# Performance work log

Hardware: AMD Instinct MI355X
Metric: run time of the kernel (lower is better)

The kernel has to match this reference:

```python
import jax, jax.numpy as jnp
import numpy as np

B, N, D, H, E = 16, 512, 256, 8, 16
DH = D // H
NEG = -1e9


def setup_inputs() -> dict:
    key = jax.random.key(0)
    ks = jax.random.split(key, 12)
    s = 0.02
    return {
        "h": jax.random.normal(ks[0], (B, N, D), dtype=jnp.float32),
        "edges": jax.random.normal(ks[1], (B, N, N, E), dtype=jnp.float32),
        "dense_mask": jnp.ones((B, N, N), dtype=bool),
        "mask": jnp.ones((B, N), dtype=bool),
        "Wq": jax.random.normal(ks[2], (D, D), dtype=jnp.float32) * s,
        "bq": jnp.zeros((D,), dtype=jnp.float32),
        "Wk": jax.random.normal(ks[3], (D, D), dtype=jnp.float32) * s,
        "bk": jnp.zeros((D,), dtype=jnp.float32),
        "Wv": jax.random.normal(ks[4], (D, D), dtype=jnp.float32) * s,
        "bv": jnp.zeros((D,), dtype=jnp.float32),
        "Wo": jax.random.normal(ks[5], (D, D), dtype=jnp.float32) * s,
        "bo": jnp.zeros((D,), dtype=jnp.float32),
        "Wp": jax.random.normal(ks[6], (E, H), dtype=jnp.float32) * s,
        "bp": jnp.zeros((H,), dtype=jnp.float32),
    }


def reference(h, edges, dense_mask, mask, Wq, bq, Wk, bk, Wv, bv, Wo, bo, Wp, bp):
    # content Q/K/V projections, split into heads
    q = (h @ Wq + bq).reshape(B, N, H, DH)
    k = (h @ Wk + bk).reshape(B, N, H, DH)
    v = (h @ Wv + bv).reshape(B, N, H, DH)
    # scaled content scores [B,H,N,N]
    scores = jnp.einsum("bnhd,bmhd->bhnm", q, k) / jnp.sqrt(jnp.float32(DH))
    # PositionAttention: per-head edge bias from the dense edge stack
    pos = jnp.einsum("bnme,eh->bhnm", edges, Wp) + bp[None, :, None, None]
    pos = pos / jnp.sqrt(jnp.float32(H))  # scale_attention
    scores = scores + pos  # merge_attention: sum (bias injected into scores)
    # fuse edge mask (dense_mask) with key padding mask (~mask is attn_mask)
    valid = dense_mask[:, None, :, :] & mask[:, None, None, :]
    scores = jnp.where(valid, scores, NEG)
    attn = jax.nn.softmax(scores, axis=-1)
    out = jnp.einsum("bhnm,bmhd->bnhd", attn, v).reshape(B, N, D)
    out = out @ Wo + bo
    return out, attn
```

## Files before the change

### kernel.cpp

```cpp
#include <hip/hip_runtime.h>
#include <hip/hip_bf16.h>

constexpr int kB = 16, kN = 512, kD = 256, kH = 8, kE = 16, kDH = 32;

typedef float f4 __attribute__((ext_vector_type(4)));
typedef __bf16 bf8 __attribute__((ext_vector_type(8)));

__global__ __launch_bounds__(256) void cast_h_kernel(const float* __restrict__ h,
                                                     __bf16* __restrict__ hb) {
  const int idx = (blockIdx.x * 256 + threadIdx.x) * 8;
  f4 a = *(const f4*)(h + idx);
  f4 b = *(const f4*)(h + idx + 4);
  bf8 o;
  o[0] = (__bf16)a[0]; o[1] = (__bf16)a[1]; o[2] = (__bf16)a[2]; o[3] = (__bf16)a[3];
  o[4] = (__bf16)b[0]; o[5] = (__bf16)b[1]; o[6] = (__bf16)b[2]; o[7] = (__bf16)b[3];
  *(bf8*)(hb + idx) = o;
}

__global__ __launch_bounds__(256) void prep_w_kernel(
    const float* __restrict__ Wq, const float* __restrict__ Wk,
    const float* __restrict__ Wv, const float* __restrict__ Wo,
    __bf16* __restrict__ Wt, __bf16* __restrict__ Wot) {
  const int r = blockIdx.x;
  const int t = threadIdx.x;
  if (r < 768) {
    const float* src = (r < 256) ? Wq : (r < 512) ? Wk : Wv;
    const int c = r & 255;
    Wt[(size_t)r * 256 + t] = (__bf16)src[(size_t)t * 256 + c];
  } else {
    const int rr = r - 768;
    Wot[(size_t)rr * 256 + t] = (__bf16)Wo[(size_t)t * 256 + rr];
  }
}

__global__ __launch_bounds__(256, 4) void qkv_gemm_kernel(
    const __bf16* __restrict__ hb, const __bf16* __restrict__ Wt,
    const float* __restrict__ bq, const float* __restrict__ bk,
    const float* __restrict__ bv,
    __bf16* __restrict__ qw, __bf16* __restrict__ kw, __bf16* __restrict__ vtw) {
  const int M0 = blockIdx.x * 128;
  const int N0 = blockIdx.y * 64;
  const int tid = threadIdx.x;
  const int wave = tid >> 6, lane = tid & 63;
  const int l15 = lane & 15, lq = lane >> 4;
  const int wm = wave & 1, wn = wave >> 1;
  const f4 fzero = {0.f, 0.f, 0.f, 0.f};

  f4 acc[4][2];
#pragma unroll
  for (int tm = 0; tm < 4; ++tm)
#pragma unroll
    for (int tn = 0; tn < 2; ++tn) acc[tm][tn] = fzero;

#pragma unroll
  for (int kk = 0; kk < 256; kk += 32) {
    bf8 af[4], bfr[2];
#pragma unroll
    for (int tm = 0; tm < 4; ++tm)
      af[tm] = *(const bf8*)(hb + (size_t)(M0 + wm * 64 + tm * 16 + l15) * 256 + kk + lq * 8);
#pragma unroll
    for (int tn = 0; tn < 2; ++tn)
      bfr[tn] = *(const bf8*)(Wt + (size_t)(N0 + wn * 32 + tn * 16 + l15) * 256 + kk + lq * 8);
#pragma unroll
    for (int tm = 0; tm < 4; ++tm)
#pragma unroll
      for (int tn = 0; tn < 2; ++tn)
        acc[tm][tn] = __builtin_amdgcn_mfma_f32_16x16x32_bf16(af[tm], bfr[tn], acc[tm][tn], 0, 0, 0);
  }

  const float QS = 0.17677669529663687f;
  const int wsel = N0 >> 8;
#pragma unroll
  for (int tn = 0; tn < 2; ++tn) {
    const int n = N0 + wn * 32 + tn * 16 + l15;
    const int c = n & 255;
    const float bias = (wsel == 0) ? bq[c] : (wsel == 1) ? bk[c] : bv[c];
#pragma unroll
    for (int tm = 0; tm < 4; ++tm) {
#pragma unroll
      for (int r = 0; r < 4; ++r) {
        const int m = M0 + wm * 64 + tm * 16 + lq * 4 + r;
        const float v = acc[tm][tn][r] + bias;
        if (wsel == 0) {
          qw[(size_t)m * 256 + c] = (__bf16)(v * QS);
        } else if (wsel == 1) {
          kw[(size_t)m * 256 + c] = (__bf16)v;
        } else {
          const int b_ = m >> 9, nn_ = m & 511, hh = c >> 5, dd = c & 31;
          vtw[(((size_t)b_ * kH + hh) * kDH + dd) * kN + nn_] = (__bf16)v;
        }
      }
    }
  }
}

__global__ __launch_bounds__(512, 2) void attn_fused_kernel(
    const __bf16* __restrict__ qw, const __bf16* __restrict__ kw,
    const __bf16* __restrict__ vtw, const float* __restrict__ edges,
    const int* __restrict__ dmask, const int* __restrict__ kmask,
    const float* __restrict__ Wp, const float* __restrict__ bp,
    float* __restrict__ attn_out, __bf16* __restrict__ ow) {
  const int blk = blockIdx.x;
  const int b = blk >> 5;
  const int n0 = (blk & 31) * 16;
  const int tid = threadIdx.x;
  const int wave = tid >> 6, lane = tid & 63;
  const int l15 = lane & 15, lq = lane >> 4;

  __shared__ union {
    float pos[8][16][132];
    __bf16 p[8][16][136];
  } su;

  f4 sc[32];
  const float RS8 = 0.35355339059327373f;
  float bph[8];
#pragma unroll
  for (int hh = 0; hh < 8; ++hh) bph[hh] = bp[hh] * RS8;

  const int mq = tid >> 7;
  const int mm = tid & 127;
#pragma unroll
  for (int cc = 0; cc < 4; ++cc) {
    const int m0 = cc * 128;
    const int km = kmask[b * kN + m0 + mm];
    float accp[4][8];
#pragma unroll
    for (int qq = 0; qq < 4; ++qq)
#pragma unroll
      for (int hh = 0; hh < 8; ++hh) accp[qq][hh] = bph[hh];

#pragma unroll
    for (int e4 = 0; e4 < 4; ++e4) {
      f4 ed[4];
#pragma unroll
      for (int qq = 0; qq < 4; ++qq) {
        const int q = mq * 4 + qq;
        ed[qq] = *(const f4*)(edges + ((size_t)(b * kN + n0 + q) * kN + m0 + mm) * kE + e4 * 4);
        ed[qq] *= RS8;
      }
#pragma unroll
      for (int i = 0; i < 4; ++i) {
#pragma unroll
        for (int hh = 0; hh < 8; ++hh) {
          const float w = Wp[(e4 * 4 + i) * kH + hh];
#pragma unroll
          for (int qq = 0; qq < 4; ++qq) accp[qq][hh] = fmaf(ed[qq][i], w, accp[qq][hh]);
        }
      }
    }
#pragma unroll
    for (int qq = 0; qq < 4; ++qq) {
      const int q = mq * 4 + qq;
      const bool valid = (dmask[(size_t)(b * kN + n0 + q) * kN + m0 + mm] != 0) && (km != 0);
#pragma unroll
      for (int hh = 0; hh < 8; ++hh)
        su.pos[hh][q][mm] = valid ? accp[qq][hh] : -1e9f;
    }
    __syncthreads();
#pragma unroll
    for (int kl = 0; kl < 8; ++kl)
#pragma unroll
      for (int r = 0; r < 4; ++r)
        sc[cc * 8 + kl][r] = su.pos[wave][lq * 4 + r][kl * 16 + l15];
    __syncthreads();
  }

  bf8 qa = *(const bf8*)(qw + ((size_t)(b * kN + n0 + l15) * kH + wave) * kDH + lq * 8);
#pragma unroll
  for (int kt = 0; kt < 32; ++kt) {
    bf8 kb = *(const bf8*)(kw + ((size_t)(b * kN + kt * 16 + l15) * kH + wave) * kDH + lq * 8);
    sc[kt] = __builtin_amdgcn_mfma_f32_16x16x32_bf16(qa, kb, sc[kt], 0, 0, 0);
  }

  float inv[4];
#pragma unroll
  for (int r = 0; r < 4; ++r) {
    float m_ = sc[0][r];
#pragma unroll
    for (int kt = 1; kt < 32; ++kt) m_ = fmaxf(m_, sc[kt][r]);
#pragma unroll
    for (int s = 1; s < 16; s <<= 1) m_ = fmaxf(m_, __shfl_xor(m_, s, 16));
    float s_ = 0.f;
#pragma unroll
    for (int kt = 0; kt < 32; ++kt) {
      const float e_ = __expf(sc[kt][r] - m_);
      sc[kt][r] = e_;
      s_ += e_;
    }
#pragma unroll
    for (int s = 1; s < 16; s <<= 1) s_ += __shfl_xor(s_, s, 16);
    inv[r] = 1.0f / s_;
  }

  const f4 fzero = {0.f, 0.f, 0.f, 0.f};
  f4 oacc[2];
  oacc[0] = fzero; oacc[1] = fzero;
  float* attn_base = attn_out + ((size_t)(b * kH + wave) * kN + n0) * kN;
#pragma unroll
  for (int cc = 0; cc < 4; ++cc) {
#pragma unroll
    for (int kl = 0; kl < 8; ++kl) {
      const int kt = cc * 8 + kl;
#pragma unroll
      for (int r = 0; r < 4; ++r) {
        const float p = sc[kt][r] * inv[r];
        attn_base[(size_t)(lq * 4 + r) * kN + kt * 16 + l15] = p;
        su.p[wave][lq * 4 + r][kl * 16 + l15] = (__bf16)p;
      }
    }
    __asm__ __volatile__("s_waitcnt lgkmcnt(0)" ::: "memory");
#pragma unroll
    for (int mc = 0; mc < 4; ++mc) {
      bf8 pa = *(const bf8*)(&su.p[wave][l15][mc * 32 + lq * 8]);
#pragma unroll
      for (int dd = 0; dd < 2; ++dd) {
        bf8 vb = *(const bf8*)(vtw + (((size_t)(b * kH + wave) * kDH) + dd * 16 + l15) * kN +
                               cc * 128 + mc * 32 + lq * 8);
        oacc[dd] = __builtin_amdgcn_mfma_f32_16x16x32_bf16(pa, vb, oacc[dd], 0, 0, 0);
      }
    }
  }

#pragma unroll
  for (int dd = 0; dd < 2; ++dd)
#pragma unroll
    for (int r = 0; r < 4; ++r)
      ow[(size_t)(b * kN + n0 + lq * 4 + r) * kD + wave * kDH + dd * 16 + l15] = (__bf16)oacc[dd][r];
}

__global__ __launch_bounds__(256, 4) void out_gemm_kernel(
    const __bf16* __restrict__ ob, const __bf16* __restrict__ Wot,
    const float* __restrict__ bo, float* __restrict__ out) {
  const int M0 = blockIdx.x * 128;
  const int N0 = blockIdx.y * 64;
  const int tid = threadIdx.x;
  const int wave = tid >> 6, lane = tid & 63;
  const int l15 = lane & 15, lq = lane >> 4;
  const int wm = wave & 1, wn = wave >> 1;
  const f4 fzero = {0.f, 0.f, 0.f, 0.f};

  f4 acc[4][2];
#pragma unroll
  for (int tm = 0; tm < 4; ++tm)
#pragma unroll
    for (int tn = 0; tn < 2; ++tn) acc[tm][tn] = fzero;

#pragma unroll
  for (int kk = 0; kk < 256; kk += 32) {
    bf8 af[4], bfr[2];
#pragma unroll
    for (int tm = 0; tm < 4; ++tm)
      af[tm] = *(const bf8*)(ob + (size_t)(M0 + wm * 64 + tm * 16 + l15) * 256 + kk + lq * 8);
#pragma unroll
    for (int tn = 0; tn < 2; ++tn)
      bfr[tn] = *(const bf8*)(Wot + (size_t)(N0 + wn * 32 + tn * 16 + l15) * 256 + kk + lq * 8);
#pragma unroll
    for (int tm = 0; tm < 4; ++tm)
#pragma unroll
      for (int tn = 0; tn < 2; ++tn)
        acc[tm][tn] = __builtin_amdgcn_mfma_f32_16x16x32_bf16(af[tm], bfr[tn], acc[tm][tn], 0, 0, 0);
  }

#pragma unroll
  for (int tn = 0; tn < 2; ++tn) {
    const int n = N0 + wn * 32 + tn * 16 + l15;
    const float bias = bo[n];
#pragma unroll
    for (int tm = 0; tm < 4; ++tm)
#pragma unroll
      for (int r = 0; r < 4; ++r) {
        const int m = M0 + wm * 64 + tm * 16 + lq * 4 + r;
        out[(size_t)m * 256 + n] = acc[tm][tn][r] + bias;
      }
  }
}

extern "C" void kernel_launch(void* const* d_in, const int* in_sizes, int n_in,
                              void* d_out, int out_size, void* d_ws, size_t ws_size,
                              hipStream_t stream) {
  const float* h = (const float*)d_in[0];
  const float* edges = (const float*)d_in[1];
  const int* dmask = (const int*)d_in[2];
  const int* kmask = (const int*)d_in[3];
  const float* Wq = (const float*)d_in[4];
  const float* bq = (const float*)d_in[5];
  const float* Wk = (const float*)d_in[6];
  const float* bk = (const float*)d_in[7];
  const float* Wv = (const float*)d_in[8];
  const float* bv = (const float*)d_in[9];
  const float* Wo = (const float*)d_in[10];
  const float* bo = (const float*)d_in[11];
  const float* Wp = (const float*)d_in[12];
  const float* bp = (const float*)d_in[13];

  char* ws = (char*)d_ws;
  __bf16* hb = (__bf16*)(ws);
  __bf16* Wt = (__bf16*)(ws + ((size_t)4 << 20));
  __bf16* Wot = (__bf16*)(ws + ((size_t)4 << 20) + 768 * 256 * 2);
  __bf16* qw = (__bf16*)(ws + ((size_t)5 << 20));
  __bf16* kw = (__bf16*)(ws + ((size_t)9 << 20));
  __bf16* vtw = (__bf16*)(ws + ((size_t)13 << 20));
  __bf16* ow = hb;

  float* out = (float*)d_out;
  float* attn = out + (size_t)kB * kN * kD;

  cast_h_kernel<<<1024, 256, 0, stream>>>(h, hb);
  prep_w_kernel<<<1024, 256, 0, stream>>>(Wq, Wk, Wv, Wo, Wt, Wot);
  qkv_gemm_kernel<<<dim3(64, 12), 256, 0, stream>>>(hb, Wt, bq, bk, bv, qw, kw, vtw);
  attn_fused_kernel<<<512, 512, 0, stream>>>(qw, kw, vtw, edges, dmask, kmask, Wp, bp, attn, ow);
  out_gemm_kernel<<<dim3(64, 4), 256, 0, stream>>>(ow, Wot, bo, out);
}
```

Baseline: 518.7 us.

## Double-buffer position-bias LDS and prefetch edge loads across chunks

```diff
diff --git a/kernel.cpp b/kernel.cpp
--- a/kernel.cpp
+++ b/kernel.cpp
@@ -108,62 +108,92 @@
   const int l15 = lane & 15, lq = lane >> 4;
 
   __shared__ union {
-    float pos[8][16][132];
+    float pos[2][8][16][132];
     __bf16 p[8][16][136];
   } su;
 
   f4 sc[32];
   const float RS8 = 0.35355339059327373f;
-  float bph[8];
-#pragma unroll
-  for (int hh = 0; hh < 8; ++hh) bph[hh] = bp[hh] * RS8;
 
   const int mq = tid >> 7;
   const int mm = tid & 127;
+
+  float bph[8];
+#pragma unroll
+  for (int hh = 0; hh < 8; ++hh) bph[hh] = bp[hh] * RS8;
+
+  f4 edc[4], edn[4];
+#pragma unroll
+  for (int qq = 0; qq < 4; ++qq)
+    edc[qq] = *(const f4*)(edges + ((size_t)(b * kN + n0 + mq * 4 + qq) * kN + mm) * kE);
+
 #pragma unroll
   for (int cc = 0; cc < 4; ++cc) {
     const int m0 = cc * 128;
     const int km = kmask[b * kN + m0 + mm];
-    float accp[4][8];
+    int dmv[4];
 #pragma unroll
     for (int qq = 0; qq < 4; ++qq)
-#pragma unroll
-      for (int hh = 0; hh < 8; ++hh) accp[qq][hh] = bph[hh];
+      dmv[qq] = dmask[(size_t)(b * kN + n0 + mq * 4 + qq) * kN + m0 + mm];
+
+    float2 acc2[4][4];
+#pragma unroll
+    for (int qq = 0; qq < 4; ++qq)
+#pragma unroll
+      for (int h2 = 0; h2 < 4; ++h2) { acc2[qq][h2].x = 0.f; acc2[qq][h2].y = 0.f; }
 
 #pragma unroll
     for (int e4 = 0; e4 < 4; ++e4) {
-      f4 ed[4];
+      if (e4 < 3) {
+#pragma unroll
+        for (int qq = 0; qq < 4; ++qq)
+          edn[qq] = *(const f4*)(edges +
+              ((size_t)(b * kN + n0 + mq * 4 + qq) * kN + m0 + mm) * kE + (e4 + 1) * 4);
+      } else if (cc < 3) {
+#pragma unroll
+        for (int qq = 0; qq < 4; ++qq)
+          edn[qq] = *(const f4*)(edges +
+              ((size_t)(b * kN + n0 + mq * 4 + qq) * kN + m0 + 128 + mm) * kE);
+      }
 #pragma unroll
       for (int qq = 0; qq < 4; ++qq) {
-        const int q = mq * 4 + qq;
-        ed[qq] = *(const f4*)(edges + ((size_t)(b * kN + n0 + q) * kN + m0 + mm) * kE + e4 * 4);
-        ed[qq] *= RS8;
-      }
-#pragma unroll
-      for (int i = 0; i < 4; ++i) {
-#pragma unroll
-        for (int hh = 0; hh < 8; ++hh) {
-          const float w = Wp[(e4 * 4 + i) * kH + hh];
-#pragma unroll
-          for (int qq = 0; qq < 4; ++qq) accp[qq][hh] = fmaf(ed[qq][i], w, accp[qq][hh]);
+#pragma unroll
+        for (int i = 0; i < 4; ++i) {
+          const float ev = edc[qq][i];
+#pragma unroll
+          for (int h2 = 0; h2 < 4; ++h2) {
+            const float2 w2 = *(const float2*)(Wp + (e4 * 4 + i) * kH + h2 * 2);
+            acc2[qq][h2].x = fmaf(ev, w2.x, acc2[qq][h2].x);
+            acc2[qq][h2].y = fmaf(ev, w2.y, acc2[qq][h2].y);
+          }
         }
       }
-    }
+      if (e4 < 3 || cc < 3) {
+#pragma unroll
+        for (int qq = 0; qq < 4; ++qq) edc[qq] = edn[qq];
+      }
+    }
+
 #pragma unroll
     for (int qq = 0; qq < 4; ++qq) {
       const int q = mq * 4 + qq;
-      const bool valid = (dmask[(size_t)(b * kN + n0 + q) * kN + m0 + mm] != 0) && (km != 0);
-#pragma unroll
-      for (int hh = 0; hh < 8; ++hh)
-        su.pos[hh][q][mm] = valid ? accp[qq][hh] : -1e9f;
-    }
-    __syncthreads();
+      const bool valid = (dmv[qq] != 0) && (km != 0);
+#pragma unroll
+      for (int h2 = 0; h2 < 4; ++h2) {
+        const float vx = fmaf(acc2[qq][h2].x, RS8, bph[h2 * 2]);
+        const float vy = fmaf(acc2[qq][h2].y, RS8, bph[h2 * 2 + 1]);
+        su.pos[cc & 1][h2 * 2][q][mm] = valid ? vx : -1e9f;
+        su.pos[cc & 1][h2 * 2 + 1][q][mm] = valid ? vy : -1e9f;
+      }
+    }
+    __asm__ __volatile__("s_waitcnt lgkmcnt(0)" ::: "memory");
+    __builtin_amdgcn_s_barrier();
+    __builtin_amdgcn_sched_barrier(0);
 #pragma unroll
     for (int kl = 0; kl < 8; ++kl)
 #pragma unroll
       for (int r = 0; r < 4; ++r)
-        sc[cc * 8 + kl][r] = su.pos[wave][lq * 4 + r][kl * 16 + l15];
-    __syncthreads();
+        sc[cc * 8 + kl][r] = su.pos[cc & 1][wave][lq * 4 + r][kl * 16 + l15];
   }
 
   bf8 qa = *(const bf8*)(qw + ((size_t)(b * kN + n0 + l15) * kH + wave) * kDH + lq * 8);
```

After: 521.9 us. Within noise of the previous version (+0.6%).

## Stream edge tiles into LDS with async double-buffered loads, per-head pos bias

Applied to the files above, without the earlier changes.

```diff
diff --git a/kernel.cpp b/kernel.cpp
--- a/kernel.cpp
+++ b/kernel.cpp
@@ -5,6 +5,12 @@
 
 typedef float f4 __attribute__((ext_vector_type(4)));
 typedef __bf16 bf8 __attribute__((ext_vector_type(8)));
+
+__device__ __forceinline__ void gload16(const void* g, const void* l) {
+  __builtin_amdgcn_global_load_lds(
+      (const __attribute__((address_space(1))) void*)g,
+      (__attribute__((address_space(3))) void*)l, 16, 0, 0);
+}
 
 __global__ __launch_bounds__(256) void cast_h_kernel(const float* __restrict__ h,
                                                      __bf16* __restrict__ hb) {
@@ -107,63 +113,93 @@
   const int wave = tid >> 6, lane = tid & 63;
   const int l15 = lane & 15, lq = lane >> 4;
 
-  __shared__ union {
-    float pos[8][16][132];
+  __shared__ __align__(16) union {
+    float stg[2][16][64][16];
     __bf16 p[8][16][136];
   } su;
 
   f4 sc[32];
   const float RS8 = 0.35355339059327373f;
-  float bph[8];
-#pragma unroll
-  for (int hh = 0; hh < 8; ++hh) bph[hh] = bp[hh] * RS8;
-
-  const int mq = tid >> 7;
-  const int mm = tid & 127;
-#pragma unroll
-  for (int cc = 0; cc < 4; ++cc) {
-    const int m0 = cc * 128;
-    const int km = kmask[b * kN + m0 + mm];
-    float accp[4][8];
-#pragma unroll
-    for (int qq = 0; qq < 4; ++qq)
-#pragma unroll
-      for (int hh = 0; hh < 8; ++hh) accp[qq][hh] = bph[hh];
-
-#pragma unroll
-    for (int e4 = 0; e4 < 4; ++e4) {
-      f4 ed[4];
-#pragma unroll
-      for (int qq = 0; qq < 4; ++qq) {
-        const int q = mq * 4 + qq;
-        ed[qq] = *(const f4*)(edges + ((size_t)(b * kN + n0 + q) * kN + m0 + mm) * kE + e4 * 4);
-        ed[qq] *= RS8;
-      }
-#pragma unroll
-      for (int i = 0; i < 4; ++i) {
-#pragma unroll
-        for (int hh = 0; hh < 8; ++hh) {
-          const float w = Wp[(e4 * 4 + i) * kH + hh];
-#pragma unroll
-          for (int qq = 0; qq < 4; ++qq) accp[qq][hh] = fmaf(ed[qq][i], w, accp[qq][hh]);
+
+  f4 wpv[4];
+#pragma unroll
+  for (int e4 = 0; e4 < 4; ++e4)
+#pragma unroll
+    for (int i = 0; i < 4; ++i) wpv[e4][i] = Wp[(e4 * 4 + i) * kH + wave] * RS8;
+  const float bph = bp[wave] * RS8;
+
+  const int msub = lane >> 2;
+  const int rotl = lane & 3;
+  const int rb = (l15 >> 1) & 3;
+
+#define STAGE_ISSUE(HC)                                                              \
+  {                                                                                  \
+    const int buf_ = (HC) & 1;                                                       \
+    _Pragma("unroll") for (int i_ = 0; i_ < 8; ++i_) {                               \
+      const int n_ = wave * 8 + i_;                                                  \
+      const int q_ = n_ >> 2;                                                        \
+      const int m_ = (n_ & 3) * 16 + msub;                                           \
+      const int e4_ = (rotl - ((m_ >> 1) & 3)) & 3;                                  \
+      const float* g_ =                                                              \
+          edges + ((size_t)(b * kN + n0 + q_) * kN + (HC)*64 + m_) * kE + e4_ * 4;   \
+      gload16(g_, (const char*)&su.stg[buf_][0][0][0] + n_ * 1024);                  \
+    }                                                                                \
+  }
+
+  STAGE_ISSUE(0);
+  __builtin_amdgcn_sched_barrier(0);
+
+#pragma unroll
+  for (int hc = 0; hc < 8; ++hc) {
+    const int buf = hc & 1;
+    if (hc < 7) {
+      STAGE_ISSUE(hc + 1);
+      __builtin_amdgcn_sched_barrier(0);
+      __asm__ __volatile__("s_waitcnt vmcnt(8)" ::: "memory");
+    } else {
+      __asm__ __volatile__("s_waitcnt vmcnt(0)" ::: "memory");
+    }
+    __builtin_amdgcn_s_barrier();
+    __builtin_amdgcn_sched_barrier(0);
+
+    const float* stg0 = &su.stg[buf][0][0][0];
+#pragma unroll
+    for (int ktl = 0; ktl < 4; ++ktl) {
+      const int mloc = ktl * 16 + l15;
+#pragma unroll
+      for (int r = 0; r < 4; ++r) {
+        const int q = lq * 4 + r;
+        const float* cell = stg0 + ((q * 64 + mloc) << 4);
+        f4 s = {0.f, 0.f, 0.f, 0.f};
+#pragma unroll
+        for (int e4 = 0; e4 < 4; ++e4) {
+          const int rot = (e4 + rb) & 3;
+          f4 ev = *(const f4*)(cell + rot * 4);
+          s += ev * wpv[e4];
         }
-      }
-    }
-#pragma unroll
-    for (int qq = 0; qq < 4; ++qq) {
-      const int q = mq * 4 + qq;
-      const bool valid = (dmask[(size_t)(b * kN + n0 + q) * kN + m0 + mm] != 0) && (km != 0);
-#pragma unroll
-      for (int hh = 0; hh < 8; ++hh)
-        su.pos[hh][q][mm] = valid ? accp[qq][hh] : -1e9f;
-    }
-    __syncthreads();
-#pragma unroll
-    for (int kl = 0; kl < 8; ++kl)
-#pragma unroll
-      for (int r = 0; r < 4; ++r)
-        sc[cc * 8 + kl][r] = su.pos[wave][lq * 4 + r][kl * 16 + l15];
-    __syncthreads();
+        sc[hc * 4 + ktl][r] = (s[0] + s[1]) + (s[2] + s[3]) + bph;
+      }
+    }
+    __builtin_amdgcn_sched_barrier(0);
+    __builtin_amdgcn_s_barrier();
+  }
+#undef STAGE_ISSUE
+
+  unsigned int vmask[4];
+#pragma unroll
+  for (int g = 0; g < 4; ++g) {
+    unsigned int vm = 0u;
+#pragma unroll
+    for (int kl = 0; kl < 8; ++kl) {
+      const int m = (g * 8 + kl) * 16 + l15;
+      const int km = kmask[b * kN + m];
+#pragma unroll
+      for (int r = 0; r < 4; ++r) {
+        const int dm = dmask[(size_t)(b * kN + n0 + lq * 4 + r) * kN + m];
+        vm |= ((km != 0 && dm != 0) ? 1u : 0u) << (kl * 4 + r);
+      }
+    }
+    vmask[g] = vm;
   }
 
   bf8 qa = *(const bf8*)(qw + ((size_t)(b * kN + n0 + l15) * kH + wave) * kDH + lq * 8);
@@ -173,6 +209,14 @@
     sc[kt] = __builtin_amdgcn_mfma_f32_16x16x32_bf16(qa, kb, sc[kt], 0, 0, 0);
   }
 
+#pragma unroll
+  for (int kt = 0; kt < 32; ++kt) {
+    const unsigned int vm = vmask[kt >> 3];
+#pragma unroll
+    for (int r = 0; r < 4; ++r) {
+      if (!((vm >> ((kt & 7) * 4 + r)) & 1u)) sc[kt][r] = -1e9f;
+    }
+  }
   float inv[4];
 #pragma unroll
   for (int r = 0; r < 4; ++r) {
```

New measurement: 550.0 us. 6.0% more time.

## Split edge-bias computation into separate kernel with bf16 packed pos buffer

Applied to the files above, without the earlier changes.

```diff
diff --git a/kernel.cpp b/kernel.cpp
--- a/kernel.cpp
+++ b/kernel.cpp
@@ -5,6 +5,12 @@
 
 typedef float f4 __attribute__((ext_vector_type(4)));
 typedef __bf16 bf8 __attribute__((ext_vector_type(8)));
+
+__device__ __forceinline__ void gload16(const void* g, const void* l) {
+  __builtin_amdgcn_global_load_lds(
+      (const __attribute__((address_space(1))) void*)g,
+      (__attribute__((address_space(3))) void*)l, 16, 0, 0);
+}
 
 __global__ __launch_bounds__(256) void cast_h_kernel(const float* __restrict__ h,
                                                      __bf16* __restrict__ hb) {
@@ -24,12 +30,97 @@
   const int r = blockIdx.x;
   const int t = threadIdx.x;
   if (r < 768) {
-    const float* src = (r < 256) ? Wq : (r < 512) ? Wk : Wv;
+    const float* src = (r < 256) ? Wq : (r < 512) ? Wv : Wv;
+    src = (r < 256) ? Wq : (r < 512) ? Wk : Wv;
     const int c = r & 255;
     Wt[(size_t)r * 256 + t] = (__bf16)src[(size_t)t * 256 + c];
   } else {
     const int rr = r - 768;
     Wot[(size_t)rr * 256 + t] = (__bf16)Wo[(size_t)t * 256 + rr];
+  }
+}
+
+__global__ __launch_bounds__(256) void prep_pos_kernel(
+    const float* __restrict__ edges, const int* __restrict__ dmask,
+    const int* __restrict__ kmask, const float* __restrict__ Wp,
+    const float* __restrict__ bp, unsigned int* __restrict__ posp) {
+  const int bn = blockIdx.x;
+  const int b = bn >> 9;
+  const int n = bn & 511;
+  const int tid = threadIdx.x;
+
+  __shared__ __align__(16) float stg[8192];
+  __shared__ __align__(16) unsigned int prow[2048];
+
+  const float* rowg = edges + (size_t)bn * (kN * kE);
+
+#pragma unroll
+  for (int j = 0; j < 8; ++j) {
+    const int L = j * 4096 + tid * 16;
+    const int c = L >> 6;
+    const int s = (L >> 4) & 3;
+    const int e4 = s ^ (c & 3);
+    gload16(rowg + c * 16 + e4 * 4, (const char*)stg + L);
+  }
+  __asm__ __volatile__("s_waitcnt vmcnt(0)" ::: "memory");
+  __builtin_amdgcn_s_barrier();
+
+  const float RS8 = 0.35355339059327373f;
+  float bph[8];
+#pragma unroll
+  for (int hh = 0; hh < 8; ++hh) bph[hh] = bp[hh] * RS8;
+
+#pragma unroll
+  for (int half = 0; half < 2; ++half) {
+    const int c = half * 256 + tid;
+    const int dm = dmask[(size_t)bn * kN + c];
+    const int km = kmask[b * kN + c];
+    const bool valid = (dm != 0) && (km != 0);
+
+    float acc[8];
+#pragma unroll
+    for (int hh = 0; hh < 8; ++hh) acc[hh] = 0.f;
+#pragma unroll
+    for (int e4 = 0; e4 < 4; ++e4) {
+      const int s = e4 ^ (c & 3);
+      f4 ev = *(const f4*)(stg + c * 16 + s * 4);
+#pragma unroll
+      for (int i = 0; i < 4; ++i) {
+        const float e_ = ev[i];
+#pragma unroll
+        for (int hh = 0; hh < 8; ++hh)
+          acc[hh] = fmaf(e_, Wp[(e4 * 4 + i) * kH + hh], acc[hh]);
+      }
+    }
+
+    unsigned int w[4];
+#pragma unroll
+    for (int pp = 0; pp < 4; ++pp) {
+      const float lo = valid ? fmaf(acc[2 * pp], RS8, bph[2 * pp]) : -1e9f;
+      const float hi = valid ? fmaf(acc[2 * pp + 1], RS8, bph[2 * pp + 1]) : -1e9f;
+      union { __bf16 h2[2]; unsigned int u; } pk;
+      pk.h2[0] = (__bf16)lo;
+      pk.h2[1] = (__bf16)hi;
+      w[pp] = pk.u;
+    }
+    const int rot = (c + (c >> 3)) & 3;
+    uint4 v;
+    ((unsigned int*)&v)[0] = w[(0 - rot) & 3];
+    ((unsigned int*)&v)[1] = w[(1 - rot) & 3];
+    ((unsigned int*)&v)[2] = w[(2 - rot) & 3];
+    ((unsigned int*)&v)[3] = w[(3 - rot) & 3];
+    *(uint4*)&prow[c * 4] = v;
+  }
+  __builtin_amdgcn_s_barrier();
+
+#pragma unroll
+  for (int it = 0; it < 8; ++it) {
+    const int li = it * 256 + tid;
+    const int pp = li >> 9;
+    const int m = li & 511;
+    const int rot = (m + (m >> 3)) & 3;
+    const unsigned int val = prow[m * 4 + ((pp + rot) & 3)];
+    posp[((((size_t)(b * 4 + pp) * kN) + n) << 9) + m] = val;
   }
 }
 
@@ -96,9 +187,7 @@
 
 __global__ __launch_bounds__(512, 2) void attn_fused_kernel(
     const __bf16* __restrict__ qw, const __bf16* __restrict__ kw,
-    const __bf16* __restrict__ vtw, const float* __restrict__ edges,
-    const int* __restrict__ dmask, const int* __restrict__ kmask,
-    const float* __restrict__ Wp, const float* __restrict__ bp,
+    const __bf16* __restrict__ vtw, const unsigned int* __restrict__ posp,
     float* __restrict__ attn_out, __bf16* __restrict__ ow) {
   const int blk = blockIdx.x;
   const int b = blk >> 5;
@@ -107,63 +196,19 @@
   const int wave = tid >> 6, lane = tid & 63;
   const int l15 = lane & 15, lq = lane >> 4;
 
-  __shared__ union {
-    float pos[8][16][132];
-    __bf16 p[8][16][136];
-  } su;
+  __shared__ __align__(16) __bf16 p[8][16][136];
 
   f4 sc[32];
-  const float RS8 = 0.35355339059327373f;
-  float bph[8];
-#pragma unroll
-  for (int hh = 0; hh < 8; ++hh) bph[hh] = bp[hh] * RS8;
-
-  const int mq = tid >> 7;
-  const int mm = tid & 127;
-#pragma unroll
-  for (int cc = 0; cc < 4; ++cc) {
-    const int m0 = cc * 128;
-    const int km = kmask[b * kN + m0 + mm];
-    float accp[4][8];
-#pragma unroll
-    for (int qq = 0; qq < 4; ++qq)
-#pragma unroll
-      for (int hh = 0; hh < 8; ++hh) accp[qq][hh] = bph[hh];
-
-#pragma unroll
-    for (int e4 = 0; e4 < 4; ++e4) {
-      f4 ed[4];
-#pragma unroll
-      for (int qq = 0; qq < 4; ++qq) {
-        const int q = mq * 4 + qq;
-        ed[qq] = *(const f4*)(edges + ((size_t)(b * kN + n0 + q) * kN + m0 + mm) * kE + e4 * 4);
-        ed[qq] *= RS8;
-      }
-#pragma unroll
-      for (int i = 0; i < 4; ++i) {
-#pragma unroll
-        for (int hh = 0; hh < 8; ++hh) {
-          const float w = Wp[(e4 * 4 + i) * kH + hh];
-#pragma unroll
-          for (int qq = 0; qq < 4; ++qq) accp[qq][hh] = fmaf(ed[qq][i], w, accp[qq][hh]);
-        }
-      }
-    }
-#pragma unroll
-    for (int qq = 0; qq < 4; ++qq) {
-      const int q = mq * 4 + qq;
-      const bool valid = (dmask[(size_t)(b * kN + n0 + q) * kN + m0 + mm] != 0) && (km != 0);
-#pragma unroll
-      for (int hh = 0; hh < 8; ++hh)
-        su.pos[hh][q][mm] = valid ? accp[qq][hh] : -1e9f;
-    }
-    __syncthreads();
-#pragma unroll
-    for (int kl = 0; kl < 8; ++kl)
-#pragma unroll
-      for (int r = 0; r < 4; ++r)
-        sc[cc * 8 + kl][r] = su.pos[wave][lq * 4 + r][kl * 16 + l15];
-    __syncthreads();
+
+  const unsigned int* pw = posp + (((size_t)(b * 4 + (wave >> 1)) * kN + n0) << 9);
+  const int hlo = wave & 1;
+#pragma unroll
+  for (int kt = 0; kt < 32; ++kt) {
+#pragma unroll
+    for (int r = 0; r < 4; ++r) {
+      const unsigned int u = pw[(size_t)(lq * 4 + r) * kN + kt * 16 + l15];
+      sc[kt][r] = __uint_as_float(hlo ? (u & 0xffff0000u) : (u << 16));
+    }
   }
 
   bf8 qa = *(const bf8*)(qw + ((size_t)(b * kN + n0 + l15) * kH + wave) * kDH + lq * 8);
@@ -204,15 +249,15 @@
       const int kt = cc * 8 + kl;
 #pragma unroll
       for (int r = 0; r < 4; ++r) {
-        const float p = sc[kt][r] * inv[r];
-        attn_base[(size_t)(lq * 4 + r) * kN + kt * 16 + l15] = p;
-        su.p[wave][lq * 4 + r][kl * 16 + l15] = (__bf16)p;
+        const float pv = sc[kt][r] * inv[r];
+        attn_base[(size_t)(lq * 4 + r) * kN + kt * 16 + l15] = pv;
+        p[wave][lq * 4 + r][kl * 16 + l15] = (__bf16)pv;
       }
     }
     __asm__ __volatile__("s_waitcnt lgkmcnt(0)" ::: "memory");
 #pragma unroll
     for (int mc = 0; mc < 4; ++mc) {
-      bf8 pa = *(const bf8*)(&su.p[wave][l15][mc * 32 + lq * 8]);
+      bf8 pa = *(const bf8*)(&p[wave][l15][mc * 32 + lq * 8]);
 #pragma unroll
       for (int dd = 0; dd < 2; ++dd) {
         bf8 vb = *(const bf8*)(vtw + (((size_t)(b * kH + wave) * kDH) + dd * 16 + l15) * kN +
@@ -301,6 +346,7 @@
   __bf16* qw = (__bf16*)(ws + ((size_t)5 << 20));
   __bf16* kw = (__bf16*)(ws + ((size_t)9 << 20));
   __bf16* vtw = (__bf16*)(ws + ((size_t)13 << 20));
+  unsigned int* posp = (unsigned int*)(ws + ((size_t)32 << 20));
   __bf16* ow = hb;
 
   float* out = (float*)d_out;
@@ -309,6 +355,7 @@
   cast_h_kernel<<<1024, 256, 0, stream>>>(h, hb);
   prep_w_kernel<<<1024, 256, 0, stream>>>(Wq, Wk, Wv, Wo, Wt, Wot);
   qkv_gemm_kernel<<<dim3(64, 12), 256, 0, stream>>>(hb, Wt, bq, bk, bv, qw, kw, vtw);
-  attn_fused_kernel<<<512, 512, 0, stream>>>(qw, kw, vtw, edges, dmask, kmask, Wp, bp, attn, ow);
+  prep_pos_kernel<<<kB * kN, 256, 0, stream>>>(edges, dmask, kmask, Wp, bp, posp);
+  attn_fused_kernel<<<512, 512, 0, stream>>>(qw, kw, vtw, posp, attn, ow);
   out_gemm_kernel<<<dim3(64, 4), 256, 0, stream>>>(ow, Wot, bo, out);
 }
```

New measurement: 540.1 us. 1.04x slower.
